# Performance work log

Hardware: AMD Instinct MI355X
Metric: run time of the kernel (lower is better)

Reference implementation:

```python
import jax, jax.numpy as jnp
import numpy as np

N_ATOMS = 8192
N_PAIRS = 65536
F = 128        # n_atombasis
R = 20         # n_radialbasis
B = 5          # graph_n_blocks
EPS = 1e-8     # stability constant


def setup_inputs() -> dict:
    key = jax.random.key(0)
    ks = jax.random.split(key, 16)
    rn = lambda k, shape, s=0.05: jax.random.normal(k, shape, dtype=jnp.float32) * s
    return {
        "features": jax.random.normal(ks[0], (N_ATOMS, F), jnp.float32),
        "distances": jax.random.uniform(ks[1], (N_PAIRS,), jnp.float32, 0.5, 5.0),
        "vectors": jax.random.normal(ks[2], (N_PAIRS, 3), jnp.float32),
        "cutoffs": jax.random.uniform(ks[3], (N_PAIRS,), jnp.float32),
        "rbfs": jax.random.normal(ks[4], (N_PAIRS, R), jnp.float32),
        "filter_W": rn(ks[5], (R, B * 3 * F)),
        "filter_b": jnp.zeros((B * 3 * F,), jnp.float32),
        "int_W1": rn(ks[6], (B, F, F)),
        "int_b1": jnp.zeros((B, F), jnp.float32),
        "int_W2": rn(ks[7], (B, F, 3 * F)),
        "int_b2": jnp.zeros((B, 3 * F), jnp.float32),
        "mix_Wv": rn(ks[8], (B, F, 2 * F)),
        "mix_W1": rn(ks[9], (B, 2 * F, F)),
        "mix_b1": jnp.zeros((B, F), jnp.float32),
        "mix_W2": rn(ks[10], (B, F, 3 * F)),
        "mix_b2": jnp.zeros((B, 3 * F), jnp.float32),
        "idx_i": jax.random.randint(ks[11], (N_PAIRS,), 0, N_ATOMS),
        "idx_j": jax.random.randint(ks[12], (N_PAIRS,), 0, N_ATOMS),
    }


def reference(features, distances, vectors, cutoffs, rbfs,
              filter_W, filter_b, int_W1, int_b1, int_W2, int_b2,
              mix_Wv, mix_W1, mix_b1, mix_W2, mix_b2, idx_i, idx_j):
    n_atoms = features.shape[0]
    # Cutoff-weighted radial filters, one (3F) chunk per block: [P, B*3F]
    descriptors = (rbfs @ filter_W + filter_b) * cutoffs[:, None]
    dir_ij = vectors / distances[:, None]                       # [P, 3]

    q = features[:, None, :]                                    # [N, 1, F]
    mu = jnp.zeros((n_atoms, 3, F), dtype=features.dtype)       # [N, 3, F]

    for b in range(B):
        # --- interaction block ---
        x = jax.nn.silu(q @ int_W1[b] + int_b1[b]) @ int_W2[b] + int_b2[b]  # [N,1,3F]
        Wij = descriptors[:, None, b * 3 * F:(b + 1) * 3 * F]               # [P,1,3F]
        xj = x[idx_j] * Wij                                                 # [P,1,3F]
        muj = mu[idx_j]                                                     # [P,3,F]
        dq, dmuR, dmumu = jnp.split(xj, 3, axis=-1)                         # [P,1,F] each
        dmu = dmuR * dir_ij[:, :, None] + dmumu * muj                       # [P,3,F]
        q = q + jax.ops.segment_sum(dq, idx_i, num_segments=n_atoms)
        mu = mu + jax.ops.segment_sum(dmu, idx_i, num_segments=n_atoms)

        # --- mixing block ---
        mu_V, mu_W = jnp.split(mu @ mix_Wv[b], 2, axis=-1)                  # [N,3,F] each
        mu_Vn = jnp.sqrt(jnp.sum(mu_V ** 2, axis=-2, keepdims=True) + EPS)  # [N,1,F]
        ctx = jnp.concatenate([q, mu_Vn], axis=-1)                          # [N,1,2F]
        y = jax.nn.silu(ctx @ mix_W1[b] + mix_b1[b]) @ mix_W2[b] + mix_b2[b]
        dq_i, dmu_i, dqmu_i = jnp.split(y, 3, axis=-1)                      # [N,1,F] each
        q = q + dq_i + dqmu_i * jnp.sum(mu_V * mu_W, axis=1, keepdims=True)
        mu = mu + dmu_i * mu_W

    return q[:, 0, :], mu
```

## Files before the change

kernel.cpp:

```cpp
#include <hip/hip_runtime.h>
#include <hip/hip_bf16.h>

#define NA 8192
#define NP 65536
#define WROW 1920

typedef short short8 __attribute__((ext_vector_type(8)));
typedef short short4v __attribute__((ext_vector_type(4)));
typedef float floatx4 __attribute__((ext_vector_type(4)));

static __device__ __forceinline__ short f2bf(float f) {
    union { float f; unsigned u; } v; v.f = f;
    unsigned r = v.u + 0x7FFF + ((v.u >> 16) & 1);
    return (short)(r >> 16);
}
static __device__ __forceinline__ float bf2f(short s) {
    union { unsigned u; float f; } v;
    v.u = ((unsigned)(unsigned short)s) << 16;
    return v.f;
}
static __device__ __forceinline__ unsigned char f2fp8(float f) {
    int p = __builtin_amdgcn_cvt_pk_fp8_f32(f, 0.f, 0, false);
    return (unsigned char)(p & 0xFF);
}
static __device__ __forceinline__ float fp82f(unsigned char b) {
    return __builtin_amdgcn_cvt_f32_fp8((int)b, 0);
}
static __device__ __forceinline__ float silu(float v) {
    return v / (1.f + __expf(-v));
}

static __device__ __forceinline__ void swz(const float* __restrict__ src,
                                           short* __restrict__ dst,
                                           int K, int N, int idx) {
    int kn = K * N;
    int b = idx / kn;
    int r = idx - b * kn;
    int tile = r >> 9, li = r & 511;
    int lane = li >> 3, bb = li & 7;
    int Kt = K >> 5;
    int nt = tile / Kt, kt = tile - nt * Kt;
    int k = kt * 32 + (lane >> 4) * 8 + bb;
    int n = nt * 16 + (lane & 15);
    dst[idx] = f2bf(src[b * kn + k * N + n]);
}

__global__ __launch_bounds__(256) void k_tconv_all(const float* __restrict__ iW1,
                                                   const float* __restrict__ iW2,
                                                   const float* __restrict__ mWv,
                                                   const float* __restrict__ mW1,
                                                   const float* __restrict__ mW2,
                                                   const float* __restrict__ fW,
                                                   short* __restrict__ W1t,
                                                   short* __restrict__ W2t,
                                                   short* __restrict__ Wvt,
                                                   short* __restrict__ mW1t,
                                                   short* __restrict__ mW2t,
                                                   short* __restrict__ fWt) {
    int idx = blockIdx.x * 256 + threadIdx.x;
    if (idx < 81920)       { swz(iW1, W1t, 128, 128, idx); return; }
    idx -= 81920;
    if (idx < 245760)      { swz(iW2, W2t, 128, 384, idx); return; }
    idx -= 245760;
    if (idx < 163840)      { swz(mWv, Wvt, 128, 256, idx); return; }
    idx -= 163840;
    if (idx < 163840)      { swz(mW1, mW1t, 256, 128, idx); return; }
    idx -= 163840;
    if (idx < 245760)      { swz(mW2, mW2t, 128, 384, idx); return; }
    idx -= 245760;
    if (idx < 61440) {
        int b = idx / 12288;
        int r = idx - b * 12288;
        int nt = r >> 9;
        int li = r & 511;
        int lane = li >> 3, bb = li & 7;
        int k = (lane >> 4) * 8 + bb;
        int n = nt * 16 + (lane & 15);
        fWt[idx] = (k < 20) ? f2bf(fW[k * WROW + b * 384 + n]) : (short)0;
    }
}

__global__ __launch_bounds__(256) void k_init(const float* __restrict__ feat,
                                              float* __restrict__ q,
                                              float* __restrict__ mu,
                                              short* __restrict__ q_bf,
                                              short* __restrict__ mu_bfA,
                                              int* __restrict__ counts,
                                              int* __restrict__ cursor,
                                              float* __restrict__ cut_csr,
                                              short* __restrict__ rbf_c) {
    int idx = blockIdx.x * 256 + threadIdx.x;
    if (idx < NA * 128) { float v = feat[idx]; q[idx] = v; q_bf[idx] = f2bf(v); }
    mu[idx] = 0.f;
    mu_bfA[idx] = 0;
    if (idx < NA) { counts[idx] = 0; cursor[idx] = 0; }
    if (idx < 16) {
        cut_csr[NP + idx] = 0.f;
        #pragma unroll
        for (int k = 0; k < 32; ++k) rbf_c[(NP + idx) * 32 + k] = 0;
    }
}

__global__ __launch_bounds__(256) void k_hist(const int* __restrict__ idx_i,
                                              int* __restrict__ counts) {
    int p = blockIdx.x * 256 + threadIdx.x;
    if (p < NP) atomicAdd(&counts[idx_i[p]], 1);
}

__global__ __launch_bounds__(1024) void k_scan(const int* __restrict__ counts,
                                               int* __restrict__ offs) {
    __shared__ int sums[1024];
    int t = threadIdx.x;
    int local[8];
    int s = 0;
    #pragma unroll
    for (int k = 0; k < 8; ++k) { local[k] = s; s += counts[t * 8 + k]; }
    sums[t] = s;
    __syncthreads();
    for (int off = 1; off < 1024; off <<= 1) {
        int v = sums[t];
        int u = (t >= off) ? sums[t - off] : 0;
        __syncthreads();
        sums[t] = v + u;
        __syncthreads();
    }
    int base = (t > 0) ? sums[t - 1] : 0;
    #pragma unroll
    for (int k = 0; k < 8; ++k) offs[t * 8 + k] = base + local[k];
    if (t == 1023) offs[NA] = sums[1023];
}

__global__ __launch_bounds__(256) void k_fillprep(const int* __restrict__ idx_i,
                                                  const int* __restrict__ idx_j,
                                                  const int* __restrict__ offs,
                                                  int* __restrict__ cursor,
                                                  const float* __restrict__ cut,
                                                  const float* __restrict__ dist,
                                                  const float* __restrict__ vec,
                                                  const float* __restrict__ rbfs,
                                                  int* __restrict__ jcsr,
                                                  float* __restrict__ cut_csr,
                                                  float4* __restrict__ dir_csr,
                                                  short* __restrict__ rbf_c) {
    int p = blockIdx.x * 256 + threadIdx.x;
    if (p >= NP) return;
    int i = idx_i[p];
    int pos = atomicAdd(&cursor[i], 1);
    int e = offs[i] + pos;
    jcsr[e] = idx_j[p];
    float c = cut[p];
    cut_csr[e] = c;
    float invd = 1.f / dist[p];
    float4 d;
    d.x = vec[p * 3 + 0] * invd;
    d.y = vec[p * 3 + 1] * invd;
    d.z = vec[p * 3 + 2] * invd;
    d.w = 0.f;
    dir_csr[e] = d;
    #pragma unroll
    for (int k = 0; k < 20; ++k) rbf_c[e * 32 + k] = f2bf(rbfs[p * 20 + k] * c);
    #pragma unroll
    for (int k = 20; k < 32; ++k) rbf_c[e * 32 + k] = 0;
}

__global__ __launch_bounds__(256) void k_x(const short* __restrict__ q_bf,
                                           const short* __restrict__ W1sw,
                                           const short* __restrict__ W2sw,
                                           const float* __restrict__ b1,
                                           const float* __restrict__ b2,
                                           unsigned char* __restrict__ x_fp8) {
    __shared__ __align__(16) short qtile[16 * 136];
    __shared__ __align__(16) short hs[16 * 136];
    int t = threadIdx.x;
    int wv = t >> 6, lane = t & 63, quad = lane >> 4, l16 = lane & 15;
    int a0 = blockIdx.x * 16;

    #pragma unroll
    for (int it = 0; it < 2; ++it) {
        int c = it * 256 + t;
        int row = c >> 5, col4 = c & 31;
        *(short4v*)(qtile + row * 136 + col4 * 4) =
            *(const short4v*)(q_bf + (a0 + row) * 128 + col4 * 4);
    }
    __syncthreads();

    floatx4 acc0 = {0.f, 0.f, 0.f, 0.f}, acc1 = {0.f, 0.f, 0.f, 0.f};
    #pragma unroll
    for (int kk = 0; kk < 4; ++kk) {
        short8 a  = *(const short8*)(qtile + l16 * 136 + kk * 32 + quad * 8);
        short8 b0 = *(const short8*)(W1sw + ((wv * 2 + 0) * 4 + kk) * 512 + lane * 8);
        short8 bq = *(const short8*)(W1sw + ((wv * 2 + 1) * 4 + kk) * 512 + lane * 8);
        acc0 = __builtin_amdgcn_mfma_f32_16x16x32_bf16(a, b0, acc0, 0, 0, 0);
        acc1 = __builtin_amdgcn_mfma_f32_16x16x32_bf16(a, bq, acc1, 0, 0, 0);
    }
    __syncthreads();
    {
        int n0 = wv * 32 + l16;
        float bia0 = b1[n0], bia1 = b1[n0 + 16];
        #pragma unroll
        for (int r = 0; r < 4; ++r) {
            int m = quad * 4 + r;
            hs[m * 136 + n0]      = f2bf(silu(acc0[r] + bia0));
            hs[m * 136 + n0 + 16] = f2bf(silu(acc1[r] + bia1));
        }
    }
    __syncthreads();
    floatx4 acc[6];
    #pragma unroll
    for (int jj = 0; jj < 6; ++jj) acc[jj] = {0.f, 0.f, 0.f, 0.f};
    #pragma unroll
    for (int kk = 0; kk < 4; ++kk) {
        short8 a = *(const short8*)(hs + l16 * 136 + kk * 32 + quad * 8);
        #pragma unroll
        for (int jj = 0; jj < 6; ++jj) {
            short8 b = *(const short8*)(W2sw + ((wv * 6 + jj) * 4 + kk) * 512 + lane * 8);
            acc[jj] = __builtin_amdgcn_mfma_f32_16x16x32_bf16(a, b, acc[jj], 0, 0, 0);
        }
    }
    #pragma unroll
    for (int jj = 0; jj < 6; ++jj) {
        int n = wv * 96 + jj * 16 + l16;
        float bia = b2[n];
        #pragma unroll
        for (int r = 0; r < 4; ++r) {
            int m = quad * 4 + r;
            x_fp8[(a0 + m) * 384 + n] = f2fp8(acc[jj][r] + bia);
        }
    }
}

__global__ __launch_bounds__(256, 6) void k_gather(const unsigned char* __restrict__ x_fp8,
                                                   const short* __restrict__ mu_bfA,
                                                   const short* __restrict__ rbf_c,
                                                   const short* __restrict__ fWt,
                                                   const float* __restrict__ fbp,
                                                   const int* __restrict__ jcsr,
                                                   const float* __restrict__ cut_csr,
                                                   const float4* __restrict__ dir_csr,
                                                   const int* __restrict__ offs,
                                                   short* __restrict__ dqg,
                                                   short* __restrict__ dmug) {
    __shared__ short dlds[16 * 392];
    __shared__ float pm[4 * 128];
    int i = blockIdx.x;
    int t = threadIdx.x;
    int h = t >> 7;
    int f = t & 127;
    int wv = t >> 6, lane = t & 63, quad = lane >> 4, l16 = lane & 15;
    int start = offs[i], end = offs[i + 1];
    float qa = 0.f, m0a = 0.f, m1a = 0.f, m2a = 0.f;

    for (int e0 = start; e0 < end; e0 += 16) {
        if (e0 > start) __syncthreads();
        short8 a = *(const short8*)(rbf_c + (e0 + l16) * 32 + quad * 8);
        float c0 = cut_csr[e0 + quad * 4 + 0];
        float c1 = cut_csr[e0 + quad * 4 + 1];
        float c2 = cut_csr[e0 + quad * 4 + 2];
        float c3 = cut_csr[e0 + quad * 4 + 3];
        #pragma unroll
        for (int nt = 0; nt < 6; ++nt) {
            int col = wv * 96 + nt * 16 + l16;
            short8 bfr = *(const short8*)(fWt + (wv * 6 + nt) * 512 + lane * 8);
            floatx4 z = {0.f, 0.f, 0.f, 0.f};
            floatx4 acc = __builtin_amdgcn_mfma_f32_16x16x32_bf16(a, bfr, z, 0, 0, 0);
            float fbv = fbp[col];
            dlds[(quad * 4 + 0) * 392 + col] = f2bf(acc[0] + fbv * c0);
            dlds[(quad * 4 + 1) * 392 + col] = f2bf(acc[1] + fbv * c1);
            dlds[(quad * 4 + 2) * 392 + col] = f2bf(acc[2] + fbv * c2);
            dlds[(quad * 4 + 3) * 392 + col] = f2bf(acc[3] + fbv * c3);
        }
        __syncthreads();
        int lim = (end < e0 + 16) ? end : (e0 + 16);
        int e = e0 + h;
        if (e < lim) {
            int jA = jcsr[e];
            float4 dirA = dir_csr[e];
            unsigned char aX0 = x_fp8[jA * 384 + f];
            unsigned char aX1 = x_fp8[jA * 384 + 128 + f];
            unsigned char aX2 = x_fp8[jA * 384 + 256 + f];
            short aU0 = mu_bfA[jA * 384 + f];
            short aU1 = mu_bfA[jA * 384 + 128 + f];
            short aU2 = mu_bfA[jA * 384 + 256 + f];
            for (; e < lim; e += 2) {
                float x0 = fp82f(aX0), x1 = fp82f(aX1), x2 = fp82f(aX2);
                float u0 = bf2f(aU0), u1 = bf2f(aU1), u2 = bf2f(aU2);
                float4 cdir = dirA;
                int en = e + 2;
                if (en < lim) {
                    int jn = jcsr[en];
                    dirA = dir_csr[en];
                    aX0 = x_fp8[jn * 384 + f];
                    aX1 = x_fp8[jn * 384 + 128 + f];
                    aX2 = x_fp8[jn * 384 + 256 + f];
                    aU0 = mu_bfA[jn * 384 + f];
                    aU1 = mu_bfA[jn * 384 + 128 + f];
                    aU2 = mu_bfA[jn * 384 + 256 + f];
                }
                int le = e - e0;
                float wa = bf2f(dlds[le * 392 + f]);
                float wb = bf2f(dlds[le * 392 + 128 + f]);
                float wc = bf2f(dlds[le * 392 + 256 + f]);
                qa += x0 * wa;
                float xb = x1 * wb;
                float xc = x2 * wc;
                m0a += xb * cdir.x + xc * u0;
                m1a += xb * cdir.y + xc * u1;
                m2a += xb * cdir.z + xc * u2;
            }
        }
    }
    if (h == 1) {
        pm[0 * 128 + f] = qa;
        pm[1 * 128 + f] = m0a;
        pm[2 * 128 + f] = m1a;
        pm[3 * 128 + f] = m2a;
    }
    __syncthreads();
    if (h == 0) {
        qa  += pm[0 * 128 + f];
        m0a += pm[1 * 128 + f];
        m1a += pm[2 * 128 + f];
        m2a += pm[3 * 128 + f];
        dqg[i * 128 + f]             = f2bf(qa);
        dmug[(i * 3 + 0) * 128 + f]  = f2bf(m0a);
        dmug[(i * 3 + 1) * 128 + f]  = f2bf(m1a);
        dmug[(i * 3 + 2) * 128 + f]  = f2bf(m2a);
    }
}

__global__ __launch_bounds__(512, 4) void k_mixx(const float* __restrict__ mu_ro,
                                                 const short* __restrict__ dmug,
                                                 const float* __restrict__ q_ro,
                                                 const short* __restrict__ dqg,
                                                 const short* __restrict__ Wvsw,
                                                 const short* __restrict__ W1sw,
                                                 const short* __restrict__ W2sw,
                                                 const float* __restrict__ b1,
                                                 const float* __restrict__ b2,
                                                 float* __restrict__ q,
                                                 float* __restrict__ mu,
                                                 short* __restrict__ mu_bfA,
                                                 const short* __restrict__ xW1sw,
                                                 const short* __restrict__ xW2sw,
                                                 const float* __restrict__ xb1,
                                                 const float* __restrict__ xb2,
                                                 unsigned char* __restrict__ x_fp8,
                                                 int do_x) {
    __shared__ __align__(16) char smem[51968];
    short* ms    = (short*)(smem);
    short* qtile = (short*)(smem + 13056);
    short* Vv    = (short*)(smem + 17408);
    short* hs    = (short*)(smem + 17408);
    short* Vw    = (short*)(smem + 30464);
    short* vnb   = (short*)(smem + 43520);
    short* sb    = (short*)(smem + 47872);
    int t = threadIdx.x;
    int wv = t >> 6, lane = t & 63, quad = lane >> 4, l16 = lane & 15;
    int a0 = blockIdx.x * 16;

    #pragma unroll
    for (int k = 0; k < 12; ++k) {
        int idx = k * 512 + t;
        int row = idx >> 7, c = idx & 127;
        int g = (a0 * 3 + row) * 128 + c;
        ms[row * 136 + c] = f2bf(mu_ro[g] + bf2f(dmug[g]));
    }
    #pragma unroll
    for (int k = 0; k < 4; ++k) {
        int idx = k * 512 + t;
        int row = idx >> 7, c = idx & 127;
        int g = (a0 + row) * 128 + c;
        qtile[row * 136 + c] = f2bf(q_ro[g] + bf2f(dqg[g]));
    }
    __syncthreads();

    {
        floatx4 acc[3][2];
        #pragma unroll
        for (int mt = 0; mt < 3; ++mt)
            #pragma unroll
            for (int nt = 0; nt < 2; ++nt) acc[mt][nt] = {0.f, 0.f, 0.f, 0.f};
        #pragma unroll
        for (int kk = 0; kk < 4; ++kk) {
            short8 a[3];
            #pragma unroll
            for (int mt = 0; mt < 3; ++mt)
                a[mt] = *(const short8*)(ms + (mt * 16 + l16) * 136 + kk * 32 + quad * 8);
            #pragma unroll
            for (int nt = 0; nt < 2; ++nt) {
                short8 b = *(const short8*)(Wvsw + ((wv * 2 + nt) * 4 + kk) * 512 + lane * 8);
                #pragma unroll
                for (int mt = 0; mt < 3; ++mt)
                    acc[mt][nt] = __builtin_amdgcn_mfma_f32_16x16x32_bf16(a[mt], b, acc[mt][nt], 0, 0, 0);
            }
        }
        __syncthreads();
        #pragma unroll
        for (int mt = 0; mt < 3; ++mt)
            #pragma unroll
            for (int nt = 0; nt < 2; ++nt)
                #pragma unroll
                for (int r = 0; r < 4; ++r) {
                    int row = mt * 16 + quad * 4 + r;
                    int col = wv * 32 + nt * 16 + l16;
                    short v = f2bf(acc[mt][nt][r]);
                    if (col < 128) Vv[row * 136 + col] = v;
                    else           Vw[row * 136 + col - 128] = v;
                }
    }
    __syncthreads();
    #pragma unroll
    for (int k = 0; k < 4; ++k) {
        int idx = k * 512 + t;
        int a = idx >> 7, c = idx & 127;
        float v0 = bf2f(Vv[(a * 3 + 0) * 136 + c]);
        float v1 = bf2f(Vv[(a * 3 + 1) * 136 + c]);
        float v2 = bf2f(Vv[(a * 3 + 2) * 136 + c]);
        float w0 = bf2f(Vw[(a * 3 + 0) * 136 + c]);
        float w1 = bf2f(Vw[(a * 3 + 1) * 136 + c]);
        float w2 = bf2f(Vw[(a * 3 + 2) * 136 + c]);
        vnb[a * 136 + c] = f2bf(sqrtf(v0 * v0 + v1 * v1 + v2 * v2 + 1e-8f));
        sb[a * 128 + c]  = f2bf(v0 * w0 + v1 * w1 + v2 * w2);
    }
    __syncthreads();
    {
        floatx4 acc0 = {0.f, 0.f, 0.f, 0.f};
        #pragma unroll
        for (int kk = 0; kk < 8; ++kk) {
            short8 a;
            if (kk < 4)
                a = *(const short8*)(qtile + l16 * 136 + kk * 32 + quad * 8);
            else
                a = *(const short8*)(vnb + l16 * 136 + (kk - 4) * 32 + quad * 8);
            short8 b0 = *(const short8*)(W1sw + (wv * 8 + kk) * 512 + lane * 8);
            acc0 = __builtin_amdgcn_mfma_f32_16x16x32_bf16(a, b0, acc0, 0, 0, 0);
        }
        __syncthreads();
        int n0 = wv * 16 + l16;
        float bia0 = b1[n0];
        #pragma unroll
        for (int r = 0; r < 4; ++r) {
            int m = quad * 4 + r;
            hs[m * 136 + n0] = f2bf(silu(acc0[r] + bia0));
        }
    }
    __syncthreads();
    {
        floatx4 accB[3];
        #pragma unroll
        for (int c = 0; c < 3; ++c) accB[c] = {0.f, 0.f, 0.f, 0.f};
        #pragma unroll
        for (int kk = 0; kk < 4; ++kk) {
            short8 a = *(const short8*)(hs + l16 * 136 + kk * 32 + quad * 8);
            #pragma unroll
            for (int c = 0; c < 3; ++c) {
                short8 b = *(const short8*)(W2sw + ((c * 8 + wv) * 4 + kk) * 512 + lane * 8);
                accB[c] = __builtin_amdgcn_mfma_f32_16x16x32_bf16(a, b, accB[c], 0, 0, 0);
            }
        }
        int co = wv * 16 + l16;
        float bq_  = b2[co];
        float bm_  = b2[128 + co];
        float bqm_ = b2[256 + co];
        #pragma unroll
        for (int r = 0; r < 4; ++r) {
            int m = quad * 4 + r;
            int ga = a0 + m;
            float dq   = accB[0][r] + bq_;
            float dmu  = accB[1][r] + bm_;
            float dqmu = accB[2][r] + bqm_;
            float sv = bf2f(sb[m * 128 + co]);
            int gq = ga * 128 + co;
            float qn = (q[gq] + bf2f(dqg[gq])) + dq + dqmu * sv;
            q[gq] = qn;
            qtile[m * 136 + co] = f2bf(qn);
            #pragma unroll
            for (int d = 0; d < 3; ++d) {
                int gm = (ga * 3 + d) * 128 + co;
                float mw = bf2f(Vw[(m * 3 + d) * 136 + co]);
                float mn = (mu[gm] + bf2f(dmug[gm])) + dmu * mw;
                mu[gm] = mn;
                mu_bfA[gm] = f2bf(mn);
            }
        }
    }
    if (!do_x) return;
    __syncthreads();
    {
        floatx4 acc0 = {0.f, 0.f, 0.f, 0.f};
        #pragma unroll
        for (int kk = 0; kk < 4; ++kk) {
            short8 a  = *(const short8*)(qtile + l16 * 136 + kk * 32 + quad * 8);
            short8 b0 = *(const short8*)(xW1sw + (wv * 4 + kk) * 512 + lane * 8);
            acc0 = __builtin_amdgcn_mfma_f32_16x16x32_bf16(a, b0, acc0, 0, 0, 0);
        }
        __syncthreads();
        int n0 = wv * 16 + l16;
        float bia0 = xb1[n0];
        #pragma unroll
        for (int r = 0; r < 4; ++r) {
            int m = quad * 4 + r;
            hs[m * 136 + n0] = f2bf(silu(acc0[r] + bia0));
        }
    }
    __syncthreads();
    {
        floatx4 acc[3];
        #pragma unroll
        for (int jj = 0; jj < 3; ++jj) acc[jj] = {0.f, 0.f, 0.f, 0.f};
        #pragma unroll
        for (int kk = 0; kk < 4; ++kk) {
            short8 a = *(const short8*)(hs + l16 * 136 + kk * 32 + quad * 8);
            #pragma unroll
            for (int jj = 0; jj < 3; ++jj) {
                short8 b = *(const short8*)(xW2sw + ((wv * 3 + jj) * 4 + kk) * 512 + lane * 8);
                acc[jj] = __builtin_amdgcn_mfma_f32_16x16x32_bf16(a, b, acc[jj], 0, 0, 0);
            }
        }
        #pragma unroll
        for (int jj = 0; jj < 3; ++jj) {
            int n = wv * 48 + jj * 16 + l16;
            float bia = xb2[n];
            #pragma unroll
            for (int r = 0; r < 4; ++r) {
                int m = quad * 4 + r;
                x_fp8[(a0 + m) * 384 + n] = f2fp8(acc[jj][r] + bia);
            }
        }
    }
}

extern "C" void kernel_launch(void* const* d_in, const int* in_sizes, int n_in,
                              void* d_out, int out_size, void* d_ws, size_t ws_size,
                              hipStream_t stream) {
    const float* feat = (const float*)d_in[0];
    const float* dist = (const float*)d_in[1];
    const float* vec  = (const float*)d_in[2];
    const float* cut  = (const float*)d_in[3];
    const float* rbfs = (const float*)d_in[4];
    const float* fW   = (const float*)d_in[5];
    const float* fb   = (const float*)d_in[6];
    const float* iW1  = (const float*)d_in[7];
    const float* ib1  = (const float*)d_in[8];
    const float* iW2  = (const float*)d_in[9];
    const float* ib2  = (const float*)d_in[10];
    const float* mWv  = (const float*)d_in[11];
    const float* mW1  = (const float*)d_in[12];
    const float* mb1  = (const float*)d_in[13];
    const float* mW2  = (const float*)d_in[14];
    const float* mb2  = (const float*)d_in[15];
    const int* idx_i  = (const int*)d_in[16];
    const int* idx_j  = (const int*)d_in[17];

    float* q  = (float*)d_out;
    float* mu = (float*)d_out + NA * 128;

    char* w = (char*)d_ws;
    unsigned char* x_fp8 = (unsigned char*)(w);
    short* dqg     = (short*)(w + 3145728);
    short* q_bf    = (short*)(w + 6291456);
    short* mu_bfA  = (short*)(w + 8388608);
    short* dmug    = (short*)(w + 14680064);
    short* W1t     = (short*)(w + 20971520);
    short* W2t     = (short*)(w + 21135360);
    short* Wvt     = (short*)(w + 21626880);
    short* mW1t    = (short*)(w + 21954560);
    short* mW2t    = (short*)(w + 22282240);
    short* fWt     = (short*)(w + 22773760);
    int*   counts  = (int*)(w + 22896640);
    int*   cursor  = (int*)(w + 22929408);
    int*   offs    = (int*)(w + 22962176);
    int*   jcsr    = (int*)(w + 23257104);
    float* cut_csr = (float*)(w + 23519248);
    float4* dir_csr= (float4*)(w + 23781456);
    short* rbf_c   = (short*)(w + 24830032);

    k_tconv_all<<<(962560 + 255) / 256, 256, 0, stream>>>(iW1, iW2, mWv, mW1, mW2, fW,
                                                          W1t, W2t, Wvt, mW1t, mW2t, fWt);
    k_init<<<NA * 384 / 256, 256, 0, stream>>>(feat, q, mu, q_bf, mu_bfA, counts, cursor,
                                               cut_csr, rbf_c);
    k_hist<<<NP / 256, 256, 0, stream>>>(idx_i, counts);
    k_scan<<<1, 1024, 0, stream>>>(counts, offs);
    k_fillprep<<<NP / 256, 256, 0, stream>>>(idx_i, idx_j, offs, cursor, cut, dist, vec,
                                             rbfs, jcsr, cut_csr, dir_csr, rbf_c);

    k_x<<<NA / 16, 256, 0, stream>>>(q_bf, W1t, W2t, ib1, ib2, x_fp8);
    for (int b = 0; b < 5; ++b) {
        int bn = (b + 1) % 5;
        k_gather<<<NA, 256, 0, stream>>>(x_fp8, mu_bfA, rbf_c, fWt + b * 12288,
                                         fb + b * 384, jcsr, cut_csr, dir_csr,
                                         offs, dqg, dmug);
        k_mixx<<<NA / 16, 512, 0, stream>>>(mu, dmug, q, dqg,
                                            Wvt + b * 32768,
                                            mW1t + b * 32768, mW2t + b * 49152,
                                            mb1 + b * 128, mb2 + b * 384,
                                            q, mu, mu_bfA,
                                            W1t + bn * 16384, W2t + bn * 49152,
                                            ib1 + bn * 128, ib2 + bn * 384,
                                            x_fp8, (b < 4) ? 1 : 0);
    }
}
```

Baseline: 417.7 us.

## Interleave fp8 x and bf16 mu into one 12-byte per-feature record for gathers

Merges the separate fp8 x buffer and bf16 mu buffer into one interleaved array, so each gathered neighbour feature is read as a single 12-byte vector load instead of six scattered scalar loads. k_x and k_mixx now write into the interleaved layout. k_mixx also drops three __syncthreads after MFMA loops and raises the launch-bounds occupancy hint from 4 to 6. Dropping the barriers risks shared-memory races if later writes overlap data other waves are still reading. The strided byte and short stores into the 12-byte records may coalesce worse on the write side.

```diff
diff --git a/kernel.cpp b/kernel.cpp
--- a/kernel.cpp
+++ b/kernel.cpp
@@ -8,6 +8,7 @@
 typedef short short8 __attribute__((ext_vector_type(8)));
 typedef short short4v __attribute__((ext_vector_type(4)));
 typedef float floatx4 __attribute__((ext_vector_type(4)));
+typedef unsigned uint3v __attribute__((ext_vector_type(3)));
 
 static __device__ __forceinline__ short f2bf(float f) {
     union { float f; unsigned u; } v; v.f = f;
@@ -84,7 +85,7 @@
                                               float* __restrict__ q,
                                               float* __restrict__ mu,
                                               short* __restrict__ q_bf,
-                                              short* __restrict__ mu_bfA,
+                                              unsigned* __restrict__ xmu_u,
                                               int* __restrict__ counts,
                                               int* __restrict__ cursor,
                                               float* __restrict__ cut_csr,
@@ -92,7 +93,7 @@
     int idx = blockIdx.x * 256 + threadIdx.x;
     if (idx < NA * 128) { float v = feat[idx]; q[idx] = v; q_bf[idx] = f2bf(v); }
     mu[idx] = 0.f;
-    mu_bfA[idx] = 0;
+    xmu_u[idx] = 0;
     if (idx < NA) { counts[idx] = 0; cursor[idx] = 0; }
     if (idx < 16) {
         cut_csr[NP + idx] = 0.f;
@@ -168,7 +169,7 @@
                                            const short* __restrict__ W2sw,
                                            const float* __restrict__ b1,
                                            const float* __restrict__ b2,
-                                           unsigned char* __restrict__ x_fp8) {
+                                           unsigned char* __restrict__ xmu) {
     __shared__ __align__(16) short qtile[16 * 136];
     __shared__ __align__(16) short hs[16 * 136];
     int t = threadIdx.x;
@@ -224,13 +225,13 @@
         #pragma unroll
         for (int r = 0; r < 4; ++r) {
             int m = quad * 4 + r;
-            x_fp8[(a0 + m) * 384 + n] = f2fp8(acc[jj][r] + bia);
-        }
-    }
-}
-
-__global__ __launch_bounds__(256, 6) void k_gather(const unsigned char* __restrict__ x_fp8,
-                                                   const short* __restrict__ mu_bfA,
+            xmu[(size_t)((a0 + m) * 128 + (n & 127)) * 12 + (n >> 7)] =
+                f2fp8(acc[jj][r] + bia);
+        }
+    }
+}
+
+__global__ __launch_bounds__(256, 6) void k_gather(const unsigned char* __restrict__ xmu,
                                                    const short* __restrict__ rbf_c,
                                                    const short* __restrict__ fWt,
                                                    const float* __restrict__ fbp,
@@ -275,27 +276,22 @@
         if (e < lim) {
             int jA = jcsr[e];
             float4 dirA = dir_csr[e];
-            unsigned char aX0 = x_fp8[jA * 384 + f];
-            unsigned char aX1 = x_fp8[jA * 384 + 128 + f];
-            unsigned char aX2 = x_fp8[jA * 384 + 256 + f];
-            short aU0 = mu_bfA[jA * 384 + f];
-            short aU1 = mu_bfA[jA * 384 + 128 + f];
-            short aU2 = mu_bfA[jA * 384 + 256 + f];
+            uint3v recA = *(const uint3v*)(xmu + (size_t)jA * 1536 + f * 12);
             for (; e < lim; e += 2) {
-                float x0 = fp82f(aX0), x1 = fp82f(aX1), x2 = fp82f(aX2);
-                float u0 = bf2f(aU0), u1 = bf2f(aU1), u2 = bf2f(aU2);
+                uint3v rec = recA;
                 float4 cdir = dirA;
                 int en = e + 2;
                 if (en < lim) {
                     int jn = jcsr[en];
                     dirA = dir_csr[en];
-                    aX0 = x_fp8[jn * 384 + f];
-                    aX1 = x_fp8[jn * 384 + 128 + f];
-                    aX2 = x_fp8[jn * 384 + 256 + f];
-                    aU0 = mu_bfA[jn * 384 + f];
-                    aU1 = mu_bfA[jn * 384 + 128 + f];
-                    aU2 = mu_bfA[jn * 384 + 256 + f];
+                    recA = *(const uint3v*)(xmu + (size_t)jn * 1536 + f * 12);
                 }
+                float x0 = fp82f((unsigned char)(rec.x & 0xFF));
+                float x1 = fp82f((unsigned char)((rec.x >> 8) & 0xFF));
+                float x2 = fp82f((unsigned char)((rec.x >> 16) & 0xFF));
+                float u0 = bf2f((short)(rec.y & 0xFFFF));
+                float u1 = bf2f((short)(rec.y >> 16));
+                float u2 = bf2f((short)(rec.z & 0xFFFF));
                 int le = e - e0;
                 float wa = bf2f(dlds[le * 392 + f]);
                 float wb = bf2f(dlds[le * 392 + 128 + f]);
@@ -328,7 +324,7 @@
     }
 }
 
-__global__ __launch_bounds__(512, 4) void k_mixx(const float* __restrict__ mu_ro,
+__global__ __launch_bounds__(512, 6) void k_mixx(const float* __restrict__ mu_ro,
                                                  const short* __restrict__ dmug,
                                                  const float* __restrict__ q_ro,
                                                  const short* __restrict__ dqg,
@@ -339,12 +335,11 @@
                                                  const float* __restrict__ b2,
                                                  float* __restrict__ q,
                                                  float* __restrict__ mu,
-                                                 short* __restrict__ mu_bfA,
+                                                 unsigned char* __restrict__ xmu,
                                                  const short* __restrict__ xW1sw,
                                                  const short* __restrict__ xW2sw,
                                                  const float* __restrict__ xb1,
                                                  const float* __restrict__ xb2,
-                                                 unsigned char* __restrict__ x_fp8,
                                                  int do_x) {
     __shared__ __align__(16) char smem[51968];
     short* ms    = (short*)(smem);
@@ -394,7 +389,6 @@
                     acc[mt][nt] = __builtin_amdgcn_mfma_f32_16x16x32_bf16(a[mt], b, acc[mt][nt], 0, 0, 0);
             }
         }
-        __syncthreads();
         #pragma unroll
         for (int mt = 0; mt < 3; ++mt)
             #pragma unroll
@@ -435,7 +429,6 @@
             short8 b0 = *(const short8*)(W1sw + (wv * 8 + kk) * 512 + lane * 8);
             acc0 = __builtin_amdgcn_mfma_f32_16x16x32_bf16(a, b0, acc0, 0, 0, 0);
         }
-        __syncthreads();
         int n0 = wv * 16 + l16;
         float bia0 = b1[n0];
         #pragma unroll
@@ -480,7 +473,7 @@
                 float mw = bf2f(Vw[(m * 3 + d) * 136 + co]);
                 float mn = (mu[gm] + bf2f(dmug[gm])) + dmu * mw;
                 mu[gm] = mn;
-                mu_bfA[gm] = f2bf(mn);
+                *(short*)(xmu + (size_t)gq * 12 + 4 + 2 * d) = f2bf(mn);
             }
         }
     }
@@ -494,7 +487,6 @@
             short8 b0 = *(const short8*)(xW1sw + (wv * 4 + kk) * 512 + lane * 8);
             acc0 = __builtin_amdgcn_mfma_f32_16x16x32_bf16(a, b0, acc0, 0, 0, 0);
         }
-        __syncthreads();
         int n0 = wv * 16 + l16;
         float bia0 = xb1[n0];
         #pragma unroll
@@ -524,7 +516,8 @@
             #pragma unroll
             for (int r = 0; r < 4; ++r) {
                 int m = quad * 4 + r;
-                x_fp8[(a0 + m) * 384 + n] = f2fp8(acc[jj][r] + bia);
+                xmu[(size_t)((a0 + m) * 128 + (n & 127)) * 12 + (n >> 7)] =
+                    f2fp8(acc[jj][r] + bia);
             }
         }
     }
@@ -556,47 +549,46 @@
     float* mu = (float*)d_out + NA * 128;
 
     char* w = (char*)d_ws;
-    unsigned char* x_fp8 = (unsigned char*)(w);
-    short* dqg     = (short*)(w + 3145728);
-    short* q_bf    = (short*)(w + 6291456);
-    short* mu_bfA  = (short*)(w + 8388608);
-    short* dmug    = (short*)(w + 14680064);
-    short* W1t     = (short*)(w + 20971520);
-    short* W2t     = (short*)(w + 21135360);
-    short* Wvt     = (short*)(w + 21626880);
-    short* mW1t    = (short*)(w + 21954560);
-    short* mW2t    = (short*)(w + 22282240);
-    short* fWt     = (short*)(w + 22773760);
-    int*   counts  = (int*)(w + 22896640);
-    int*   cursor  = (int*)(w + 22929408);
-    int*   offs    = (int*)(w + 22962176);
-    int*   jcsr    = (int*)(w + 23257104);
-    float* cut_csr = (float*)(w + 23519248);
-    float4* dir_csr= (float4*)(w + 23781456);
-    short* rbf_c   = (short*)(w + 24830032);
+    unsigned char* xmu = (unsigned char*)(w);
+    short* dqg     = (short*)(w + 12582912);
+    short* q_bf    = (short*)(w + 14680064);
+    short* dmug    = (short*)(w + 16777216);
+    short* W1t     = (short*)(w + 23068672);
+    short* W2t     = (short*)(w + 23232512);
+    short* Wvt     = (short*)(w + 23724032);
+    short* mW1t    = (short*)(w + 24051712);
+    short* mW2t    = (short*)(w + 24379392);
+    short* fWt     = (short*)(w + 24870912);
+    int*   counts  = (int*)(w + 24993792);
+    int*   cursor  = (int*)(w + 25026560);
+    int*   offs    = (int*)(w + 25059328);
+    int*   jcsr    = (int*)(w + 25092112);
+    float* cut_csr = (float*)(w + 25354256);
+    float4* dir_csr= (float4*)(w + 25616464);
+    short* rbf_c   = (short*)(w + 26665040);
 
     k_tconv_all<<<(962560 + 255) / 256, 256, 0, stream>>>(iW1, iW2, mWv, mW1, mW2, fW,
                                                           W1t, W2t, Wvt, mW1t, mW2t, fWt);
-    k_init<<<NA * 384 / 256, 256, 0, stream>>>(feat, q, mu, q_bf, mu_bfA, counts, cursor,
-                                               cut_csr, rbf_c);
+    k_init<<<NA * 384 / 256, 256, 0, stream>>>(feat, q, mu, q_bf, (unsigned*)xmu,
+                                               counts, cursor, cut_csr, rbf_c);
     k_hist<<<NP / 256, 256, 0, stream>>>(idx_i, counts);
     k_scan<<<1, 1024, 0, stream>>>(counts, offs);
     k_fillprep<<<NP / 256, 256, 0, stream>>>(idx_i, idx_j, offs, cursor, cut, dist, vec,
                                              rbfs, jcsr, cut_csr, dir_csr, rbf_c);
 
-    k_x<<<NA / 16, 256, 0, stream>>>(q_bf, W1t, W2t, ib1, ib2, x_fp8);
+    k_x<<<NA / 16, 256, 0, stream>>>(q_bf, W1t, W2t, ib1, ib2, xmu);
     for (int b = 0; b < 5; ++b) {
         int bn = (b + 1) % 5;
-        k_gather<<<NA, 256, 0, stream>>>(x_fp8, mu_bfA, rbf_c, fWt + b * 12288,
+        k_gather<<<NA, 256, 0, stream>>>(xmu, rbf_c, fWt + b * 12288,
                                          fb + b * 384, jcsr, cut_csr, dir_csr,
                                          offs, dqg, dmug);
         k_mixx<<<NA / 16, 512, 0, stream>>>(mu, dmug, q, dqg,
                                             Wvt + b * 32768,
                                             mW1t + b * 32768, mW2t + b * 49152,
                                             mb1 + b * 128, mb2 + b * 384,
-                                            q, mu, mu_bfA,
+                                            q, mu, xmu,
                                             W1t + bn * 16384, W2t + bn * 49152,
                                             ib1 + bn * 128, ib2 + bn * 384,
-                                            x_fp8, (b < 4) ? 1 : 0);
-    }
-}
+                                            (b < 4) ? 1 : 0);
+    }
+}
```

Measured after the change: 415.6 us. Within noise of the previous version (-0.5%).
